# Kernel optimization log

Measured on AMD Instinct MI355X. Metric: run time of the kernel, lower is better.

Reference implementation:

```python
import jax, jax.numpy as jnp
import numpy as np

H = 256      # hidden_size
L = 20       # max_length
V = 29       # output_size (vocab)
LAT = H + 8


def setup_inputs() -> dict:
    key = jax.random.key(0)
    ks = jax.random.split(key, 20)
    s = 0.05
    return {
        "input_tensor": jax.random.randint(ks[0], (1,), 0, V),
        "hidden": jax.random.normal(ks[1], (1, 1, H), dtype=jnp.float32),
        "encoder_outputs": jax.random.normal(ks[2], (L, H), dtype=jnp.float32),
        "cond": jax.random.randint(ks[3], (2,), 0, 4),
        "is_head": 1,
        # parameters (PyTorch Linear convention: weight [out, in])
        "emb": jax.random.normal(ks[4], (V, H), dtype=jnp.float32) * s,
        "w_l2d": jax.random.normal(ks[5], (H, LAT), dtype=jnp.float32) * s,
        "b_l2d": jnp.zeros((H,), dtype=jnp.float32),
        "w_attn": jax.random.normal(ks[6], (L, 2 * H), dtype=jnp.float32) * s,
        "b_attn": jnp.zeros((L,), dtype=jnp.float32),
        "w_comb": jax.random.normal(ks[7], (H, 2 * H), dtype=jnp.float32) * s,
        "b_comb": jnp.zeros((H,), dtype=jnp.float32),
        "w_ih": jax.random.normal(ks[8], (3 * H, H), dtype=jnp.float32) * s,
        "w_hh": jax.random.normal(ks[9], (3 * H, H), dtype=jnp.float32) * s,
        "b_ih": jnp.zeros((3 * H,), dtype=jnp.float32),
        "b_hh": jnp.zeros((3 * H,), dtype=jnp.float32),
        "w_out": jax.random.normal(ks[10], (V, H), dtype=jnp.float32) * s,
        "b_out": jnp.zeros((V,), dtype=jnp.float32),
    }


def gru_cell(x, h, w_ih, w_hh, b_ih, b_hh):
    # x, h: [1, H]; PyTorch GRU gate order: r, z, n
    gi = x @ w_ih.T + b_ih
    gh = h @ w_hh.T + b_hh
    ir, iz, inn = jnp.split(gi, 3, axis=-1)
    hr, hz, hn = jnp.split(gh, 3, axis=-1)
    r = jax.nn.sigmoid(ir + hr)
    z = jax.nn.sigmoid(iz + hz)
    n = jnp.tanh(inn + r * hn)
    return (1.0 - z) * n + z * h


def reference(input_tensor, hidden, encoder_outputs, cond, is_head,
              emb, w_l2d, b_l2d, w_attn, b_attn, w_comb, b_comb,
              w_ih, w_hh, b_ih, b_hh, w_out, b_out):
    if is_head:
        c = jnp.concatenate([jax.nn.one_hot(cond[0], 4),
                             jax.nn.one_hot(cond[1], 4)]).astype(hidden.dtype)  # [8]
        hidden = jnp.concatenate([hidden, c[None, None, :]], axis=2)  # [1,1,H+8]
        hidden = hidden @ w_l2d.T + b_l2d                              # [1,1,H]
    embedded = emb[input_tensor].reshape(1, 1, -1)                     # [1,1,H] (dropout: eval mode)
    attn_in = jnp.concatenate([embedded[0], hidden[0]], axis=1)        # [1,2H]
    attn_weights = jax.nn.softmax(attn_in @ w_attn.T + b_attn, axis=1) # [1,L]
    attn_applied = attn_weights @ encoder_outputs                      # [1,H]
    output = jnp.concatenate([embedded[0], attn_applied], axis=1)      # [1,2H]
    output = jax.nn.relu(output @ w_comb.T + b_comb)                   # [1,H]
    h_new = gru_cell(output, hidden[0], w_ih, w_hh, b_ih, b_hh)        # [1,H]
    logits = jax.nn.log_softmax(h_new @ w_out.T + b_out, axis=1)       # [1,V]
    return logits, h_new[None], attn_weights
```

## Files before the change

### kernel.cpp

```cpp
#include <hip/hip_runtime.h>
#include <hip/hip_bf16.h>

#define H 256
#define L 20
#define V 29
#define LAT 264
#define NBLK 129
#define NTHR 256
#define PZN 0xAAAAAAAAu


__device__ __forceinline__ float wave_sum(float v) {
#pragma unroll
    for (int o = 32; o > 0; o >>= 1) v += __shfl_down(v, o, 64);
    return v;
}

__device__ __forceinline__ void stws(float* p, float v) {
    __hip_atomic_store(p, v, __ATOMIC_RELAXED, __HIP_MEMORY_SCOPE_AGENT);
}

__device__ __forceinline__ float pollf(const float* p) {
    union { unsigned u; float f; } v;
    long spins = 0;
    for (;;) {
        v.u = __hip_atomic_load((const unsigned*)p, __ATOMIC_RELAXED,
                                __HIP_MEMORY_SCOPE_AGENT);
        if (v.u != PZN) break;
        __builtin_amdgcn_s_sleep(1);
        if (++spins > 5000000L) break;
    }
    return v.f;
}

__device__ __forceinline__ void copy_g2l4(float* dst, const float* src, int nfloats) {
    const float4* s4 = (const float4*)src;
    float4* d4 = (float4*)dst;
    const int n4 = nfloats >> 2;
    for (int i = threadIdx.x; i < n4; i += NTHR) d4[i] = s4[i];
}

__global__ __launch_bounds__(NTHR) void decoder_step(
    const int* inp, const float* hidden, const float* enc,
    const int* cond, const int* is_head,
    const float* emb, const float* w_l2d, const float* b_l2d,
    const float* w_attn, const float* b_attn,
    const float* w_comb, const float* b_comb,
    const float* w_ih, const float* w_hh,
    const float* b_ih, const float* b_hh,
    const float* w_out, const float* b_out,
    float* ws, float* out)
{
    extern __shared__ float sm[];
    const int b = blockIdx.x;
    const int t = threadIdx.x;
    const int wave = t >> 6, lane = t & 63;

    if (b < 32) {
        const int c0 = b * 8;
        if (is_head[0]) {
            float x0 = hidden[lane],       x1 = hidden[64 + lane];
            float x2 = hidden[128 + lane], x3 = hidden[192 + lane];
            float x4 = 0.f;
            if (lane < 8) {
                int c = (lane < 4) ? cond[0] : cond[1];
                x4 = (c == (lane & 3)) ? 1.f : 0.f;
            }
#pragma unroll
            for (int q = 0; q < 2; ++q) {
                int r = c0 + wave * 2 + q;
                const float* wr = w_l2d + r * LAT;
                float s = wr[lane] * x0 + wr[64 + lane] * x1
                        + wr[128 + lane] * x2 + wr[192 + lane] * x3;
                if (lane < 8) s += wr[256 + lane] * x4;
                s = wave_sum(s);
                if (lane == 0) stws(&ws[r], s + b_l2d[r]);
            }
        } else {
            if (t < 8) stws(&ws[c0 + t], hidden[c0 + t]);
        }

    } else if (b < 64) {
        const int k = b - 32, r0 = k * 8;
        float* wah  = sm;
        float* encl = sm + 5120;
        float* wcl  = sm + 10240;
        float* xatt = sm + 14336;
        float* bc   = sm + 14848;
        float* lge  = sm + 14864;
        float* lg   = sm + 14896;
        float* aw   = sm + 14928;
        for (int i = t; i < L * 64; i += NTHR) {
            int r = i >> 6, q = i & 63;
            ((float4*)wah)[r * 64 + q] = ((const float4*)(w_attn + r * 2 * H + H))[q];
        }
        copy_g2l4(encl, enc, L * H);
        copy_g2l4(wcl, w_comb + r0 * 2 * H, 8 * 2 * H);
        xatt[t] = emb[inp[0] * H + t];
        if (t < 8) bc[t] = b_comb[r0 + t];
        __syncthreads();
        for (int r = wave; r < L; r += 4) {
            float s = 0.f;
#pragma unroll
            for (int j = lane; j < H; j += 64) s += w_attn[r * 2 * H + j] * xatt[j];
            s = wave_sum(s);
            if (lane == 0) lge[r] = s + b_attn[r];
        }
        xatt[H + t] = pollf(ws + t);
        __syncthreads();
        for (int r = wave; r < L; r += 4) {
            float s = 0.f;
#pragma unroll
            for (int j = lane; j < H; j += 64) s += wah[r * H + j] * xatt[H + j];
            s = wave_sum(s);
            if (lane == 0) lg[r] = lge[r] + s;
        }
        __syncthreads();
        if (wave == 0) {
            float v = (lane < L) ? lg[lane] : -1e30f;
            float m = v;
#pragma unroll
            for (int o = 32; o > 0; o >>= 1) m = fmaxf(m, __shfl_xor(m, o, 64));
            float e = (lane < L) ? __expf(v - m) : 0.f;
            float ssum = e;
#pragma unroll
            for (int o = 32; o > 0; o >>= 1) ssum += __shfl_xor(ssum, o, 64);
            if (lane < L) {
                float a = e / ssum;
                aw[lane] = a;
                if (k == 0) out[V + H + lane] = a;
            }
        }
        __syncthreads();
        {
            float s = 0.f;
#pragma unroll
            for (int l = 0; l < L; ++l) s += aw[l] * encl[l * H + t];
            xatt[H + t] = s;
        }
        __syncthreads();
#pragma unroll
        for (int q = 0; q < 2; ++q) {
            int r = wave * 2 + q;
            float s = 0.f;
#pragma unroll
            for (int j = lane; j < 2 * H; j += 64) s += wcl[r * 2 * H + j] * xatt[j];
            s = wave_sum(s);
            if (lane == 0) stws(&ws[512 + r0 + r], fmaxf(s + bc[r], 0.f));
        }

    } else if (b < 96) {
        const int k = b - 64, c0 = k * 8;
        float* wi  = sm;
        float* xo  = sm + 6144;
        float* bb  = sm + 6400;
        float* gis = sm + 6424;
        copy_g2l4(wi,          w_ih + c0 * H,           8 * H);
        copy_g2l4(wi + 8 * H,  w_ih + (H + c0) * H,     8 * H);
        copy_g2l4(wi + 16 * H, w_ih + (2 * H + c0) * H, 8 * H);
        if (t < 24) { int g = t >> 3, i = t & 7; bb[t] = b_ih[g * H + c0 + i]; }
        xo[t] = pollf(ws + 512 + t);
        __syncthreads();
#pragma unroll
        for (int q = 0; q < 6; ++q) {
            int m = wave * 6 + q;
            float s = 0.f;
#pragma unroll
            for (int j = lane; j < H; j += 64) s += wi[m * H + j] * xo[j];
            s = wave_sum(s);
            if (lane == 0) gis[m] = s + bb[m];
        }
        __syncthreads();
        if (t < 8) {
            const float* ghp = ws + 1536 + k * 24;
            float ghr = pollf(ghp + t);
            float ghz = pollf(ghp + 8 + t);
            float ghn = pollf(ghp + 16 + t);
            float h2  = pollf(ws + c0 + t);
            float r = 1.f / (1.f + __expf(-(gis[t] + ghr)));
            float z = 1.f / (1.f + __expf(-(gis[8 + t] + ghz)));
            float n = tanhf(gis[16 + t] + r * ghn);
            float h = (1.f - z) * n + z * h2;
            out[V + c0 + t] = h;
            stws(&ws[768 + c0 + t], h);
        }

    } else if (b < 128) {
        const int k = b - 96, c0 = k * 8;
        float* w  = sm;
        float* xh = sm + 6144;
        float* bb = sm + 6400;
        copy_g2l4(w,          w_hh + c0 * H,           8 * H);
        copy_g2l4(w + 8 * H,  w_hh + (H + c0) * H,     8 * H);
        copy_g2l4(w + 16 * H, w_hh + (2 * H + c0) * H, 8 * H);
        if (t < 24) { int g = t >> 3, i = t & 7; bb[t] = b_hh[g * H + c0 + i]; }
        xh[t] = pollf(ws + t);
        __syncthreads();
#pragma unroll
        for (int q = 0; q < 6; ++q) {
            int m = wave * 6 + q;
            float s = 0.f;
#pragma unroll
            for (int j = lane; j < H; j += 64) s += w[m * H + j] * xh[j];
            s = wave_sum(s);
            if (lane == 0) stws(&ws[1536 + k * 24 + m], s + bb[m]);
        }

    } else {
        float* wo = sm;
        float* bo = sm + 7424;
        float* hn = sm + 7456;
        float* lg = sm + 7712;
        copy_g2l4(wo, w_out, V * H);
        if (t < V) bo[t] = b_out[t];
        hn[t] = pollf(ws + 768 + t);
        __syncthreads();
        for (int r = wave; r < V; r += 4) {
            float s = 0.f;
#pragma unroll
            for (int j = lane; j < H; j += 64) s += wo[r * H + j] * hn[j];
            s = wave_sum(s);
            if (lane == 0) lg[r] = s + bo[r];
        }
        __syncthreads();
        if (wave == 0) {
            float v = (lane < V) ? lg[lane] : -1e30f;
            float m = v;
#pragma unroll
            for (int o = 32; o > 0; o >>= 1) m = fmaxf(m, __shfl_xor(m, o, 64));
            float e = (lane < V) ? __expf(v - m) : 0.f;
            float s2 = e;
#pragma unroll
            for (int o = 32; o > 0; o >>= 1) s2 += __shfl_xor(s2, o, 64);
            float ls = logf(s2);
            if (lane < V) out[lane] = v - m - ls;
        }
    }
}

extern "C" void kernel_launch(void* const* d_in, const int* in_sizes, int n_in,
                              void* d_out, int out_size, void* d_ws, size_t ws_size,
                              hipStream_t stream) {
    const int* inp      = (const int*)d_in[0];
    const float* hidden = (const float*)d_in[1];
    const float* enc    = (const float*)d_in[2];
    const int* cond     = (const int*)d_in[3];
    const int* is_head  = (const int*)d_in[4];
    const float* emb    = (const float*)d_in[5];
    const float* w_l2d  = (const float*)d_in[6];
    const float* b_l2d  = (const float*)d_in[7];
    const float* w_attn = (const float*)d_in[8];
    const float* b_attn = (const float*)d_in[9];
    const float* w_comb = (const float*)d_in[10];
    const float* b_comb = (const float*)d_in[11];
    const float* w_ih   = (const float*)d_in[12];
    const float* w_hh   = (const float*)d_in[13];
    const float* b_ih   = (const float*)d_in[14];
    const float* b_hh   = (const float*)d_in[15];
    const float* w_out  = (const float*)d_in[16];
    const float* b_out  = (const float*)d_in[17];

    float* ws = (float*)d_ws;
    float* out = (float*)d_out;

    const size_t smem = 14960 * sizeof(float);
    decoder_step<<<NBLK, NTHR, smem, stream>>>(
        inp, hidden, enc, cond, is_head, emb, w_l2d, b_l2d, w_attn, b_attn,
        w_comb, b_comb, w_ih, w_hh, b_ih, b_hh, w_out, b_out, ws, out);
}
```

Before: 105.3 us.

## Merge GRU hidden-gate blocks into input-gate blocks to drop cross-block handoff

```diff
diff --git a/kernel.cpp b/kernel.cpp
--- a/kernel.cpp
+++ b/kernel.cpp
@@ -5,7 +5,7 @@
 #define L 20
 #define V 29
 #define LAT 264
-#define NBLK 129
+#define NBLK 97
 #define NTHR 256
 #define PZN 0xAAAAAAAAu
 
@@ -151,59 +151,55 @@
 
     } else if (b < 96) {
         const int k = b - 64, c0 = k * 8;
-        float* wi  = sm;
-        float* xo  = sm + 6144;
-        float* bb  = sm + 6400;
-        float* gis = sm + 6424;
+        float* wh  = sm;
+        float* wi  = sm + 6144;
+        float* xh  = sm + 12288;
+        float* xo  = sm + 12544;
+        float* bbh = sm + 12800;
+        float* bbi = sm + 12824;
+        float* ghs = sm + 12848;
+        float* gis = sm + 12872;
+        copy_g2l4(wh,          w_hh + c0 * H,           8 * H);
+        copy_g2l4(wh + 8 * H,  w_hh + (H + c0) * H,     8 * H);
+        copy_g2l4(wh + 16 * H, w_hh + (2 * H + c0) * H, 8 * H);
         copy_g2l4(wi,          w_ih + c0 * H,           8 * H);
         copy_g2l4(wi + 8 * H,  w_ih + (H + c0) * H,     8 * H);
         copy_g2l4(wi + 16 * H, w_ih + (2 * H + c0) * H, 8 * H);
-        if (t < 24) { int g = t >> 3, i = t & 7; bb[t] = b_ih[g * H + c0 + i]; }
-        xo[t] = pollf(ws + 512 + t);
+        if (t < 24) { int g = t >> 3, i = t & 7; bbh[t] = b_hh[g * H + c0 + i]; }
+        if (t >= 32 && t < 56) {
+            int u = t - 32, g = u >> 3, i = u & 7;
+            bbi[u] = b_ih[g * H + c0 + i];
+        }
+        xh[t] = pollf(ws + t);
         __syncthreads();
 #pragma unroll
         for (int q = 0; q < 6; ++q) {
             int m = wave * 6 + q;
             float s = 0.f;
 #pragma unroll
+            for (int j = lane; j < H; j += 64) s += wh[m * H + j] * xh[j];
+            s = wave_sum(s);
+            if (lane == 0) ghs[m] = s + bbh[m];
+        }
+        xo[t] = pollf(ws + 512 + t);
+        __syncthreads();
+#pragma unroll
+        for (int q = 0; q < 6; ++q) {
+            int m = wave * 6 + q;
+            float s = 0.f;
+#pragma unroll
             for (int j = lane; j < H; j += 64) s += wi[m * H + j] * xo[j];
             s = wave_sum(s);
-            if (lane == 0) gis[m] = s + bb[m];
+            if (lane == 0) gis[m] = s + bbi[m];
         }
         __syncthreads();
         if (t < 8) {
-            const float* ghp = ws + 1536 + k * 24;
-            float ghr = pollf(ghp + t);
-            float ghz = pollf(ghp + 8 + t);
-            float ghn = pollf(ghp + 16 + t);
-            float h2  = pollf(ws + c0 + t);
-            float r = 1.f / (1.f + __expf(-(gis[t] + ghr)));
-            float z = 1.f / (1.f + __expf(-(gis[8 + t] + ghz)));
-            float n = tanhf(gis[16 + t] + r * ghn);
-            float h = (1.f - z) * n + z * h2;
+            float r = 1.f / (1.f + __expf(-(gis[t] + ghs[t])));
+            float z = 1.f / (1.f + __expf(-(gis[8 + t] + ghs[8 + t])));
+            float n = tanhf(gis[16 + t] + r * ghs[16 + t]);
+            float h = (1.f - z) * n + z * xh[c0 + t];
             out[V + c0 + t] = h;
             stws(&ws[768 + c0 + t], h);
-        }
-
-    } else if (b < 128) {
-        const int k = b - 96, c0 = k * 8;
-        float* w  = sm;
-        float* xh = sm + 6144;
-        float* bb = sm + 6400;
-        copy_g2l4(w,          w_hh + c0 * H,           8 * H);
-        copy_g2l4(w + 8 * H,  w_hh + (H + c0) * H,     8 * H);
-        copy_g2l4(w + 16 * H, w_hh + (2 * H + c0) * H, 8 * H);
-        if (t < 24) { int g = t >> 3, i = t & 7; bb[t] = b_hh[g * H + c0 + i]; }
-        xh[t] = pollf(ws + t);
-        __syncthreads();
-#pragma unroll
-        for (int q = 0; q < 6; ++q) {
-            int m = wave * 6 + q;
-            float s = 0.f;
-#pragma unroll
-            for (int j = lane; j < H; j += 64) s += w[m * H + j] * xh[j];
-            s = wave_sum(s);
-            if (lane == 0) stws(&ws[1536 + k * 24 + m], s + bb[m]);
         }
 
     } else {
```

Measured after the change: 104.3 us. No clear change (-1.0%).
